# Optimization experiments

Hardware: AMD Instinct MI355X
Metric: run time of the kernel (lower is better)

The kernel has to match this reference:

```python
import jax, jax.numpy as jnp
import numpy as np

NUM_HEADS = 8
WEIGHTS_DIM = 512
INPUT_DIM = 512
D_HEAD = WEIGHTS_DIM // NUM_HEADS


def setup_inputs() -> dict:
    key = jax.random.key(0)
    ks = jax.random.split(key, 9)
    B, S, D = 4, 2048, INPUT_DIM
    s_in = 1.0 / np.sqrt(D)
    s_w = 1.0 / np.sqrt(WEIGHTS_DIM)
    return {
        "x": jax.random.normal(ks[0], (B, S, D), dtype=jnp.float32),
        "Wq": jax.random.normal(ks[1], (D, WEIGHTS_DIM), dtype=jnp.float32) * s_in,
        "bq": jnp.zeros((WEIGHTS_DIM,), dtype=jnp.float32),
        "Wk": jax.random.normal(ks[2], (D, WEIGHTS_DIM), dtype=jnp.float32) * s_in,
        "bk": jnp.zeros((WEIGHTS_DIM,), dtype=jnp.float32),
        "Wv": jax.random.normal(ks[3], (D, WEIGHTS_DIM), dtype=jnp.float32) * s_in,
        "bv": jnp.zeros((WEIGHTS_DIM,), dtype=jnp.float32),
        "Wh": jax.random.normal(ks[4], (WEIGHTS_DIM, D), dtype=jnp.float32) * s_w,
        "bh": jnp.zeros((D,), dtype=jnp.float32),
    }


def _split_heads(t):
    # [B, S, Dm] -> [B, H, S, d_head]
    B, S, _ = t.shape
    return t.reshape(B, S, NUM_HEADS, D_HEAD).transpose(0, 2, 1, 3)


def reference(x, Wq, bq, Wk, bk, Wv, bv, Wh, bh):
    q = _split_heads(x @ Wq + bq)
    k = _split_heads(x @ Wk + bk)
    v = _split_heads(x @ Wv + bv)
    scale = 1.0 / jnp.sqrt(jnp.float32(D_HEAD))
    scores = jnp.einsum("bhqd,bhkd->bhqk", q, k) * scale  # [B,H,S,S]
    weights = jax.nn.softmax(scores, axis=-1)
    attn = jnp.einsum("bhqk,bhkd->bhqd", weights, v)
    B, H, S, d = attn.shape
    concat = attn.transpose(0, 2, 1, 3).reshape(B, S, H * d)
    return concat @ Wh + bh
```

## Files before the change

### kernel.cpp

```cpp
#include <hip/hip_runtime.h>
#include <stdint.h>

#define NB  4
#define SS  2048
#define DD  512
#define HH  8
#define DHH 64
#define MM  (NB * SS)

typedef __attribute__((ext_vector_type(8))) short bf16x8;
typedef __attribute__((ext_vector_type(4))) float f32x4;
typedef __attribute__((ext_vector_type(16))) float f32x16;
typedef __attribute__((ext_vector_type(4))) short s16x4;

union fu32 { float f; unsigned u; };
union pfu  { uint4 u; bf16x8 v; };

static __device__ __forceinline__ short f2bf(float f) {
  fu32 a; a.f = f;
  unsigned u = a.u;
  return (short)((u + 0x7fffu + ((u >> 16) & 1u)) >> 16);
}
static __device__ __forceinline__ float bf2f(short s) {
  fu32 t; t.u = ((unsigned)(unsigned short)s) << 16;
  return t.f;
}

static __device__ __forceinline__ unsigned cvt_pk_bf16(float lo, float hi) {
  unsigned r;
  asm("v_cvt_pk_bf16_f32 %0, %1, %2" : "=v"(r) : "v"(lo), "v"(hi));
  return r;
}
static __device__ __forceinline__ void permlane32_swap(unsigned& a, unsigned& b) {
  asm("v_permlane32_swap_b32 %0, %1" : "+v"(a), "+v"(b));
}

static __device__ __forceinline__ void async16(const void* g, void* l) {
  __builtin_amdgcn_global_load_lds(
      (__attribute__((address_space(1))) unsigned*)(void*)g,
      (__attribute__((address_space(3))) unsigned*)l, 16, 0, 0);
}

__global__ __launch_bounds__(256) void prep_kernel(
    const float* __restrict__ x, short* __restrict__ xb,
    const float* __restrict__ W0, const float* __restrict__ W1,
    const float* __restrict__ W2, const float* __restrict__ W3,
    short* __restrict__ T0, short* __restrict__ T1,
    short* __restrict__ T2, short* __restrict__ T3) {
  const int bid = blockIdx.x, tid = threadIdx.x;
  if (bid < 2048) {
    int i = (bid * 256 + tid) * 8;
    float4 v0 = *(const float4*)(x + i);
    float4 v1 = *(const float4*)(x + i + 4);
    bf16x8 o;
    o[0] = f2bf(v0.x); o[1] = f2bf(v0.y); o[2] = f2bf(v0.z); o[3] = f2bf(v0.w);
    o[4] = f2bf(v1.x); o[5] = f2bf(v1.y); o[6] = f2bf(v1.z); o[7] = f2bf(v1.w);
    *(bf16x8*)(xb + i) = o;
  } else {
    int z = bid - 2048;
    int widx = z >> 6, rem = z & 63;
    const float* W = widx == 0 ? W0 : widx == 1 ? W1 : widx == 2 ? W2 : W3;
    short*       T = widx == 0 ? T0 : widx == 1 ? T1 : widx == 2 ? T2 : T3;
    int n  = (rem & 7) * 64 + (tid & 63);
    int k0 = (rem >> 3) * 64 + (tid >> 6) * 16;
    bf16x8 t0, t1;
#pragma unroll
    for (int j = 0; j < 8; ++j) t0[j] = f2bf(W[(size_t)(k0 + j) * DD + n]);
#pragma unroll
    for (int j = 0; j < 8; ++j) t1[j] = f2bf(W[(size_t)(k0 + 8 + j) * DD + n]);
    *(bf16x8*)(T + (size_t)n * DD + k0)     = t0;
    *(bf16x8*)(T + (size_t)n * DD + k0 + 8) = t1;
  }
}

__global__ __launch_bounds__(256, 4) void gemm_qkv_kernel(
    const short* __restrict__ A, const short* __restrict__ Bt,
    const float* __restrict__ bq, const float* __restrict__ bk,
    const float* __restrict__ bv, short* __restrict__ qout,
    short* __restrict__ kout, short* __restrict__ vtout, float qscale) {
  __shared__ __align__(16) short a_sh[64 * 64];
  __shared__ __align__(16) short b_sh[128 * 64];
  const int tid  = threadIdx.x;
  const int w    = tid >> 6, lane = tid & 63, quad = lane >> 4, l16 = lane & 15;
  const int m0   = blockIdx.y * 64, n0 = blockIdx.x * 128;
  const int mw   = (w >> 1) * 32,   nw = (w & 1) * 64;
  const int rw   = lane >> 3, seg = lane & 7, gs = seg ^ rw;
  const int sxz  = l16 & 7;

  f32x4 acc[2][4];
#pragma unroll
  for (int i = 0; i < 2; ++i)
#pragma unroll
    for (int j = 0; j < 4; ++j) acc[i][j] = {0.f, 0.f, 0.f, 0.f};

  for (int kt = 0; kt < DD; kt += 64) {
    __syncthreads();
    {
      const short* ga = A  + (size_t)(m0 + w * 16 + rw) * DD + kt + gs * 8;
      const short* gb = Bt + (size_t)(n0 + w * 32 + rw) * DD + kt + gs * 8;
#pragma unroll
      for (int i = 0; i < 2; ++i)
        async16(ga + (size_t)i * 8 * DD, &a_sh[(w * 16 + i * 8) * 64]);
#pragma unroll
      for (int i = 0; i < 4; ++i)
        async16(gb + (size_t)i * 8 * DD, &b_sh[(w * 32 + i * 8) * 64]);
    }
    __syncthreads();
#pragma unroll
    for (int ks = 0; ks < 2; ++ks) {
      const int so = ((ks * 4 + quad) ^ sxz) * 8;
      bf16x8 af[2], bfr[4];
#pragma unroll
      for (int mt = 0; mt < 2; ++mt)
        af[mt] = *(const bf16x8*)&a_sh[(mw + mt * 16 + l16) * 64 + so];
#pragma unroll
      for (int nt = 0; nt < 4; ++nt)
        bfr[nt] = *(const bf16x8*)&b_sh[(nw + nt * 16 + l16) * 64 + so];
#pragma unroll
      for (int mt = 0; mt < 2; ++mt)
#pragma unroll
        for (int nt = 0; nt < 4; ++nt)
          acc[mt][nt] = __builtin_amdgcn_mfma_f32_16x16x32_bf16(
              af[mt], bfr[nt], acc[mt][nt], 0, 0, 0);
    }
  }

#pragma unroll
  for (int nt = 0; nt < 4; ++nt) {
    const int n   = n0 + nw + nt * 16 + l16;
    const int sg  = n >> 9, n9 = n & 511, h = n9 >> 6, d = n & 63;
    const float bval = (sg == 0 ? bq : sg == 1 ? bk : bv)[n9];
    const float scl  = (sg == 0) ? qscale : 1.0f;
#pragma unroll
    for (int mt = 0; mt < 2; ++mt) {
      const int mb = m0 + mw + mt * 16 + quad * 4;
      const int bi = mb >> 11, s = mb & (SS - 1);
      if (sg == 2) {
        s16x4 pk;
#pragma unroll
        for (int r = 0; r < 4; ++r) pk[r] = f2bf(acc[mt][nt][r] + bval);
        *(s16x4*)&vtout[((size_t)(bi * HH + h) * DHH + d) * SS + s] = pk;
      } else {
        short* o = (sg == 0) ? qout : kout;
        const size_t base = ((size_t)(bi * HH + h) * SS + s) * DHH + d;
#pragma unroll
        for (int r = 0; r < 4; ++r)
          o[base + (size_t)r * DHH] = f2bf((acc[mt][nt][r] + bval) * scl);
      }
    }
  }
}

__global__ __launch_bounds__(256, 2) void attn_kernel(
    const short* __restrict__ Qa, const short* __restrict__ Ka,
    const short* __restrict__ Vt, short* __restrict__ Op0,
    short* __restrict__ Op1, float* __restrict__ lpw) {
  __shared__ __align__(16) short k_sh[2][64 * 64];
  __shared__ __align__(16) short vt_sh[2][64 * 64];

  const int tid  = threadIdx.x;
  const int w    = tid >> 6, lane = tid & 63;
  const int l32  = lane & 31, hl = lane >> 5;
  const int n    = blockIdx.x;
  const int grp  = (n & 7) * 8 + (n >> 6);
  const int qt_b = (n >> 3) & 7;
  const int half = grp & 1, h = (grp >> 1) & 7, b = grp >> 4;
  const int q0   = qt_b * 256;
  const int rw = lane >> 3, seg = lane & 7, gs = seg ^ rw;
  const size_t base = (size_t)(b * HH + h) * SS * DHH;
  const short* Qg = Qa + base + (size_t)(q0 + w * 64) * DHH;
  const short* Kg = Ka + base;
  const short* Vg = Vt + base;

  bf16x8 qf[2][4];
#pragma unroll
  for (int qx = 0; qx < 2; ++qx)
#pragma unroll
    for (int ds = 0; ds < 4; ++ds)
      qf[qx][ds] = *(const bf16x8*)(Qg + (size_t)(qx * 32 + l32) * DHH + ds * 16 + hl * 8);

  bf16x8 ones;
#pragma unroll
  for (int j = 0; j < 8; ++j) ones[j] = (short)0x3F80;

  f32x16 o_acc[2][2];
  f32x16 l_acc[2];
#pragma unroll
  for (int i = 0; i < 16; ++i) {
    o_acc[0][0][i] = 0.f; o_acc[0][1][i] = 0.f;
    o_acc[1][0][i] = 0.f; o_acc[1][1][i] = 0.f;
    l_acc[0][i] = 0.f; l_acc[1][i] = 0.f;
  }

  const int kstart = half * (SS / 2);
  const int kend   = kstart + SS / 2;

  auto stage = [&](int bsel, int kb) {
    const short* gk = Kg + (size_t)(kb + w * 16 + rw) * DHH + gs * 8;
#pragma unroll
    for (int i = 0; i < 2; ++i)
      async16(gk + (size_t)i * 8 * DHH, &k_sh[bsel][(w * 16 + i * 8) * 64]);
#pragma unroll
    for (int i = 0; i < 2; ++i) {
      const int d = w * 16 + i * 8 + rw;
      async16(Vg + (size_t)d * SS + kb + gs * 8,
              &vt_sh[bsel][(w * 16 + i * 8) * 64]);
    }
  };

  stage(0, kstart);
  __syncthreads();
  int cur = 0;

  for (int kb = kstart; kb < kend; kb += 64) {
    if (kb + 64 < kend) stage(cur ^ 1, kb + 64);

#pragma unroll
    for (int ck = 0; ck < 2; ++ck) {
      const int krow = ck * 32 + l32;
      bf16x8 kf[4];
#pragma unroll
      for (int ds = 0; ds < 4; ++ds) {
        const int sseg = (ds * 2 + hl) ^ (krow & 7);
        kf[ds] = *(const bf16x8*)&k_sh[cur][krow * 64 + sseg * 8];
      }
      f32x16 sarr[2];
#pragma unroll
      for (int qx = 0; qx < 2; ++qx) {
#pragma unroll
        for (int i = 0; i < 16; ++i) sarr[qx][i] = 0.f;
      }
      __builtin_amdgcn_s_setprio(1);
#pragma unroll
      for (int ds = 0; ds < 4; ++ds) {
        sarr[0] = __builtin_amdgcn_mfma_f32_32x32x16_bf16(kf[ds], qf[0][ds], sarr[0], 0, 0, 0);
        sarr[1] = __builtin_amdgcn_mfma_f32_32x32x16_bf16(kf[ds], qf[1][ds], sarr[1], 0, 0, 0);
      }
      __builtin_amdgcn_s_setprio(0);

      pfu a[2][2];
#pragma unroll
      for (int qx = 0; qx < 2; ++qx) {
#pragma unroll
        for (int i = 0; i < 16; ++i) sarr[qx][i] = __builtin_amdgcn_exp2f(sarr[qx][i]);
        unsigned wpk[8];
#pragma unroll
        for (int i = 0; i < 8; ++i)
          wpk[i] = cvt_pk_bf16(sarr[qx][2 * i], sarr[qx][2 * i + 1]);
        permlane32_swap(wpk[0], wpk[2]);
        permlane32_swap(wpk[1], wpk[3]);
        permlane32_swap(wpk[4], wpk[6]);
        permlane32_swap(wpk[5], wpk[7]);
        a[qx][0].u.x = wpk[0]; a[qx][0].u.y = wpk[1];
        a[qx][0].u.z = wpk[2]; a[qx][0].u.w = wpk[3];
        a[qx][1].u.x = wpk[4]; a[qx][1].u.y = wpk[5];
        a[qx][1].u.z = wpk[6]; a[qx][1].u.w = wpk[7];
      }

      __builtin_amdgcn_s_setprio(1);
      l_acc[0] = __builtin_amdgcn_mfma_f32_32x32x16_bf16(a[0][0].v, ones, l_acc[0], 0, 0, 0);
      l_acc[0] = __builtin_amdgcn_mfma_f32_32x32x16_bf16(a[0][1].v, ones, l_acc[0], 0, 0, 0);
      l_acc[1] = __builtin_amdgcn_mfma_f32_32x32x16_bf16(a[1][0].v, ones, l_acc[1], 0, 0, 0);
      l_acc[1] = __builtin_amdgcn_mfma_f32_32x32x16_bf16(a[1][1].v, ones, l_acc[1], 0, 0, 0);

#pragma unroll
      for (int dt = 0; dt < 2; ++dt) {
        const int drow = dt * 32 + l32;
#pragma unroll
        for (int ks = 0; ks < 2; ++ks) {
          const int sseg = (ck * 4 + ks * 2 + hl) ^ (drow & 7);
          bf16x8 vf = *(const bf16x8*)&vt_sh[cur][drow * 64 + sseg * 8];
          o_acc[0][dt] = __builtin_amdgcn_mfma_f32_32x32x16_bf16(
              ks == 0 ? a[0][0].v : a[0][1].v, vf, o_acc[0][dt], 0, 0, 0);
          o_acc[1][dt] = __builtin_amdgcn_mfma_f32_32x32x16_bf16(
              ks == 0 ? a[1][0].v : a[1][1].v, vf, o_acc[1][dt], 0, 0, 0);
        }
      }
      __builtin_amdgcn_s_setprio(0);
    }

    __syncthreads();
    cur ^= 1;
  }

  short* Op = half ? Op1 : Op0;
#pragma unroll
  for (int qx = 0; qx < 2; ++qx) {
#pragma unroll
    for (int r = 0; r < 16; ++r) {
      const int qg = q0 + w * 64 + qx * 32 + (r & 3) + 8 * (r >> 2) + 4 * hl;
      const size_t row = (size_t)(b * HH + h) * SS + qg;
      if (l32 == 0)
        lpw[(size_t)half * (NB * HH * SS) + row] = l_acc[qx][r];
      const float inv = __builtin_amdgcn_rcpf(l_acc[qx][r]);
#pragma unroll
      for (int dt = 0; dt < 2; ++dt)
        Op[row * DHH + dt * 32 + l32] = f2bf(o_acc[qx][dt][r] * inv);
    }
  }
}

__global__ void attn_combine_kernel(const short* __restrict__ Op0,
                                    const short* __restrict__ Op1,
                                    const float* __restrict__ lpw,
                                    short* __restrict__ aws) {
  int idx  = blockIdx.x * 256 + threadIdx.x;
  int dsg  = idx & 7;
  int row  = idx >> 3;
  int q    = row & (SS - 1);
  int bh   = row >> 11, h = bh & 7, b = bh >> 3;
  float l1 = lpw[row], l2 = lpw[NB * HH * SS + row];
  float inv = 1.f / (l1 + l2);
  float w1 = l1 * inv, w2 = l2 * inv;
  bf16x8 a = *(const bf16x8*)&Op0[(size_t)row * DHH + dsg * 8];
  bf16x8 c = *(const bf16x8*)&Op1[(size_t)row * DHH + dsg * 8];
  bf16x8 o;
#pragma unroll
  for (int j = 0; j < 8; ++j) o[j] = f2bf(w1 * bf2f(a[j]) + w2 * bf2f(c[j]));
  *(bf16x8*)&aws[((size_t)(b * SS + q)) * DD + h * DHH + dsg * 8] = o;
}

__global__ __launch_bounds__(256, 4) void gemm_proj_kernel(
    const short* __restrict__ A, const short* __restrict__ Bt,
    const float* __restrict__ bias, float* __restrict__ out) {
  __shared__ __align__(16) short a_sh[64 * 64];
  __shared__ __align__(16) short b_sh[64 * 64];
  const int tid = threadIdx.x;
  const int w   = tid >> 6, lane = tid & 63, quad = lane >> 4, l16 = lane & 15;
  const int m0  = blockIdx.y * 64, n0 = blockIdx.x * 64;
  const int mw  = (w >> 1) * 32, nw = (w & 1) * 32;
  const int rw  = lane >> 3, seg = lane & 7, gs = seg ^ rw;
  const int sxz = l16 & 7;

  f32x4 acc[2][2];
#pragma unroll
  for (int i = 0; i < 2; ++i)
#pragma unroll
    for (int j = 0; j < 2; ++j) acc[i][j] = {0.f, 0.f, 0.f, 0.f};

  for (int kt = 0; kt < DD; kt += 64) {
    __syncthreads();
    {
      const short* ga = A  + (size_t)(m0 + w * 16 + rw) * DD + kt + gs * 8;
      const short* gb = Bt + (size_t)(n0 + w * 16 + rw) * DD + kt + gs * 8;
#pragma unroll
      for (int i = 0; i < 2; ++i) {
        async16(ga + (size_t)i * 8 * DD, &a_sh[(w * 16 + i * 8) * 64]);
        async16(gb + (size_t)i * 8 * DD, &b_sh[(w * 16 + i * 8) * 64]);
      }
    }
    __syncthreads();
#pragma unroll
    for (int ks = 0; ks < 2; ++ks) {
      const int so = ((ks * 4 + quad) ^ sxz) * 8;
      bf16x8 af0 = *(const bf16x8*)&a_sh[(mw + l16) * 64 + so];
      bf16x8 af1 = *(const bf16x8*)&a_sh[(mw + 16 + l16) * 64 + so];
#pragma unroll
      for (int nt = 0; nt < 2; ++nt) {
        bf16x8 bfr = *(const bf16x8*)&b_sh[(nw + nt * 16 + l16) * 64 + so];
        acc[0][nt] = __builtin_amdgcn_mfma_f32_16x16x32_bf16(af0, bfr, acc[0][nt], 0, 0, 0);
        acc[1][nt] = __builtin_amdgcn_mfma_f32_16x16x32_bf16(af1, bfr, acc[1][nt], 0, 0, 0);
      }
    }
  }

#pragma unroll
  for (int nt = 0; nt < 2; ++nt) {
    const int   n  = n0 + nw + nt * 16 + l16;
    const float bv = bias[n];
#pragma unroll
    for (int mt = 0; mt < 2; ++mt)
#pragma unroll
      for (int r = 0; r < 4; ++r) {
        const int m = m0 + mw + mt * 16 + quad * 4 + r;
        out[(size_t)m * DD + n] = acc[mt][nt][r] + bv;
      }
  }
}

extern "C" void kernel_launch(void* const* d_in, const int* in_sizes, int n_in,
                              void* d_out, int out_size, void* d_ws, size_t ws_size,
                              hipStream_t stream) {
  (void)in_sizes; (void)n_in; (void)out_size; (void)ws_size;
  const float* x  = (const float*)d_in[0];
  const float* Wq = (const float*)d_in[1];
  const float* bq = (const float*)d_in[2];
  const float* Wk = (const float*)d_in[3];
  const float* bk = (const float*)d_in[4];
  const float* Wv = (const float*)d_in[5];
  const float* bv = (const float*)d_in[6];
  const float* Wh = (const float*)d_in[7];
  const float* bh = (const float*)d_in[8];

  short* ws  = (short*)d_ws;
  short* xb  = ws;
  short* wqt = xb  + (size_t)MM * DD;
  short* wkt = wqt + (size_t)DD * DD;
  short* wvt = wkt + (size_t)DD * DD;
  short* wht = wvt + (size_t)DD * DD;
  short* qws = wht + (size_t)DD * DD;
  short* kws = qws + (size_t)MM * DD;
  short* vws = kws + (size_t)MM * DD;
  short* aws = vws + (size_t)MM * DD;
  short* op1 = aws + (size_t)MM * DD;
  float* lpw = (float*)(op1 + (size_t)MM * DD);

  hipLaunchKernelGGL(prep_kernel, dim3(2048 + 256), dim3(256), 0, stream,
                     x, xb, Wq, Wk, Wv, Wh, wqt, wkt, wvt, wht);

  const float qscale = 1.4426950408889634f / 8.0f;
  hipLaunchKernelGGL(gemm_qkv_kernel, dim3(12, 128), dim3(256), 0, stream,
                     xb, wqt, bq, bk, bv, qws, kws, vws, qscale);

  hipLaunchKernelGGL(attn_kernel, dim3(512), dim3(256), 0, stream,
                     qws, kws, vws, xb, op1, lpw);
  hipLaunchKernelGGL(attn_combine_kernel, dim3(NB * HH * SS * 8 / 256), dim3(256), 0, stream,
                     xb, op1, lpw, aws);

  hipLaunchKernelGGL(gemm_proj_kernel, dim3(8, 128), dim3(256), 0, stream,
                     aws, wht, bh, (float*)d_out);
}
```

Measured before the change: 166.3 us.

## Split keys across waves within block and fuse split-K combine into attention

Restructures attention so each block handles 64 queries and its four waves each process a quarter of the key range. K/V tiles are read directly from global memory instead of being staged through double-buffered LDS. The partial outputs and row sums are reduced through shared memory, which removes the separate combine kernel and its intermediate buffers. The row-sum MFMAs against a ones vector are replaced with scalar accumulation. The risks are that K/V reuse now depends on cache rather than LDS, and the in-block reduction adds extra LDS traffic and register pressure, with occupancy hinted at 3 blocks per CU.

```diff
diff --git a/kernel.cpp b/kernel.cpp
--- a/kernel.cpp
+++ b/kernel.cpp
@@ -151,24 +151,22 @@
   }
 }
 
-__global__ __launch_bounds__(256, 2) void attn_kernel(
+__global__ __launch_bounds__(256, 3) void attn_kernel(
     const short* __restrict__ Qa, const short* __restrict__ Ka,
-    const short* __restrict__ Vt, short* __restrict__ Op0,
-    short* __restrict__ Op1, float* __restrict__ lpw) {
-  __shared__ __align__(16) short k_sh[2][64 * 64];
-  __shared__ __align__(16) short vt_sh[2][64 * 64];
-
-  const int tid  = threadIdx.x;
-  const int w    = tid >> 6, lane = tid & 63;
-  const int l32  = lane & 31, hl = lane >> 5;
-  const int n    = blockIdx.x;
-  const int grp  = (n & 7) * 8 + (n >> 6);
-  const int qt_b = (n >> 3) & 7;
-  const int half = grp & 1, h = (grp >> 1) & 7, b = grp >> 4;
-  const int q0   = qt_b * 256;
-  const int rw = lane >> 3, seg = lane & 7, gs = seg ^ rw;
+    const short* __restrict__ Vt, short* __restrict__ aws) {
+  __shared__ float Rsh[2][64 * 68];
+  __shared__ float l_sh[4][64];
+
+  const int tid = threadIdx.x;
+  const int w   = tid >> 6, lane = tid & 63;
+  const int l32 = lane & 31, hl = lane >> 5;
+  const int n  = blockIdx.x;
+  const int bh = (n & 7) * 4 + (n >> 8);
+  const int qt = (n >> 3) & 31;
+  const int h  = bh & 7, b = bh >> 3;
+  const int q0 = qt * 64;
   const size_t base = (size_t)(b * HH + h) * SS * DHH;
-  const short* Qg = Qa + base + (size_t)(q0 + w * 64) * DHH;
+  const short* Qg = Qa + base;
   const short* Kg = Ka + base;
   const short* Vg = Vt + base;
 
@@ -177,147 +175,122 @@
   for (int qx = 0; qx < 2; ++qx)
 #pragma unroll
     for (int ds = 0; ds < 4; ++ds)
-      qf[qx][ds] = *(const bf16x8*)(Qg + (size_t)(qx * 32 + l32) * DHH + ds * 16 + hl * 8);
-
-  bf16x8 ones;
-#pragma unroll
-  for (int j = 0; j < 8; ++j) ones[j] = (short)0x3F80;
+      qf[qx][ds] = *(const bf16x8*)(Qg + (size_t)(q0 + qx * 32 + l32) * DHH + ds * 16 + hl * 8);
 
   f32x16 o_acc[2][2];
-  f32x16 l_acc[2];
 #pragma unroll
   for (int i = 0; i < 16; ++i) {
     o_acc[0][0][i] = 0.f; o_acc[0][1][i] = 0.f;
     o_acc[1][0][i] = 0.f; o_acc[1][1][i] = 0.f;
-    l_acc[0][i] = 0.f; l_acc[1][i] = 0.f;
-  }
-
-  const int kstart = half * (SS / 2);
-  const int kend   = kstart + SS / 2;
-
-  auto stage = [&](int bsel, int kb) {
-    const short* gk = Kg + (size_t)(kb + w * 16 + rw) * DHH + gs * 8;
-#pragma unroll
-    for (int i = 0; i < 2; ++i)
-      async16(gk + (size_t)i * 8 * DHH, &k_sh[bsel][(w * 16 + i * 8) * 64]);
-#pragma unroll
-    for (int i = 0; i < 2; ++i) {
-      const int d = w * 16 + i * 8 + rw;
-      async16(Vg + (size_t)d * SS + kb + gs * 8,
-              &vt_sh[bsel][(w * 16 + i * 8) * 64]);
-    }
-  };
-
-  stage(0, kstart);
+  }
+  float lsum0 = 0.f, lsum1 = 0.f;
+
+  const int k0 = w * (SS / 4);
+
+#pragma unroll 2
+  for (int kc = 0; kc < 16; ++kc) {
+    const int kb = k0 + kc * 32;
+    bf16x8 kf[4];
+#pragma unroll
+    for (int ds = 0; ds < 4; ++ds)
+      kf[ds] = *(const bf16x8*)(Kg + (size_t)(kb + l32) * DHH + ds * 16 + hl * 8);
+
+    f32x16 s0, s1;
+#pragma unroll
+    for (int i = 0; i < 16; ++i) { s0[i] = 0.f; s1[i] = 0.f; }
+    __builtin_amdgcn_s_setprio(1);
+#pragma unroll
+    for (int ds = 0; ds < 4; ++ds) {
+      s0 = __builtin_amdgcn_mfma_f32_32x32x16_bf16(kf[ds], qf[0][ds], s0, 0, 0, 0);
+      s1 = __builtin_amdgcn_mfma_f32_32x32x16_bf16(kf[ds], qf[1][ds], s1, 0, 0, 0);
+    }
+    __builtin_amdgcn_s_setprio(0);
+
+    bf16x8 vf[2][2];
+#pragma unroll
+    for (int dt = 0; dt < 2; ++dt)
+#pragma unroll
+      for (int ks = 0; ks < 2; ++ks)
+        vf[dt][ks] = *(const bf16x8*)(Vg + (size_t)(dt * 32 + l32) * SS + kb + ks * 16 + hl * 8);
+
+    pfu a[2][2];
+#pragma unroll
+    for (int qx = 0; qx < 2; ++qx) {
+      f32x16& s = qx ? s1 : s0;
+#pragma unroll
+      for (int i = 0; i < 16; ++i) {
+        s[i] = __builtin_amdgcn_exp2f(s[i]);
+        if (qx) lsum1 += s[i]; else lsum0 += s[i];
+      }
+      unsigned wpk[8];
+#pragma unroll
+      for (int i = 0; i < 8; ++i) wpk[i] = cvt_pk_bf16(s[2 * i], s[2 * i + 1]);
+      permlane32_swap(wpk[0], wpk[2]);
+      permlane32_swap(wpk[1], wpk[3]);
+      permlane32_swap(wpk[4], wpk[6]);
+      permlane32_swap(wpk[5], wpk[7]);
+      a[qx][0].u.x = wpk[0]; a[qx][0].u.y = wpk[1];
+      a[qx][0].u.z = wpk[2]; a[qx][0].u.w = wpk[3];
+      a[qx][1].u.x = wpk[4]; a[qx][1].u.y = wpk[5];
+      a[qx][1].u.z = wpk[6]; a[qx][1].u.w = wpk[7];
+    }
+
+    __builtin_amdgcn_s_setprio(1);
+#pragma unroll
+    for (int dt = 0; dt < 2; ++dt)
+#pragma unroll
+      for (int ks = 0; ks < 2; ++ks) {
+        o_acc[0][dt] = __builtin_amdgcn_mfma_f32_32x32x16_bf16(
+            a[0][ks].v, vf[dt][ks], o_acc[0][dt], 0, 0, 0);
+        o_acc[1][dt] = __builtin_amdgcn_mfma_f32_32x32x16_bf16(
+            a[1][ks].v, vf[dt][ks], o_acc[1][dt], 0, 0, 0);
+      }
+    __builtin_amdgcn_s_setprio(0);
+  }
+
+  lsum0 += __shfl_xor(lsum0, 32);
+  lsum1 += __shfl_xor(lsum1, 32);
+  if (hl == 0) { l_sh[w][l32] = lsum0; l_sh[w][32 + l32] = lsum1; }
+
+  if (w < 2) {
+#pragma unroll
+    for (int qx = 0; qx < 2; ++qx)
+#pragma unroll
+      for (int dt = 0; dt < 2; ++dt)
+#pragma unroll
+        for (int r = 0; r < 16; ++r) {
+          const int qrow = qx * 32 + (r & 3) + 8 * (r >> 2) + 4 * hl;
+          Rsh[w][qrow * 68 + dt * 32 + l32] = o_acc[qx][dt][r];
+        }
+  }
   __syncthreads();
-  int cur = 0;
-
-  for (int kb = kstart; kb < kend; kb += 64) {
-    if (kb + 64 < kend) stage(cur ^ 1, kb + 64);
-
-#pragma unroll
-    for (int ck = 0; ck < 2; ++ck) {
-      const int krow = ck * 32 + l32;
-      bf16x8 kf[4];
-#pragma unroll
-      for (int ds = 0; ds < 4; ++ds) {
-        const int sseg = (ds * 2 + hl) ^ (krow & 7);
-        kf[ds] = *(const bf16x8*)&k_sh[cur][krow * 64 + sseg * 8];
-      }
-      f32x16 sarr[2];
-#pragma unroll
-      for (int qx = 0; qx < 2; ++qx) {
-#pragma unroll
-        for (int i = 0; i < 16; ++i) sarr[qx][i] = 0.f;
-      }
-      __builtin_amdgcn_s_setprio(1);
-#pragma unroll
-      for (int ds = 0; ds < 4; ++ds) {
-        sarr[0] = __builtin_amdgcn_mfma_f32_32x32x16_bf16(kf[ds], qf[0][ds], sarr[0], 0, 0, 0);
-        sarr[1] = __builtin_amdgcn_mfma_f32_32x32x16_bf16(kf[ds], qf[1][ds], sarr[1], 0, 0, 0);
-      }
-      __builtin_amdgcn_s_setprio(0);
-
-      pfu a[2][2];
-#pragma unroll
-      for (int qx = 0; qx < 2; ++qx) {
-#pragma unroll
-        for (int i = 0; i < 16; ++i) sarr[qx][i] = __builtin_amdgcn_exp2f(sarr[qx][i]);
-        unsigned wpk[8];
-#pragma unroll
-        for (int i = 0; i < 8; ++i)
-          wpk[i] = cvt_pk_bf16(sarr[qx][2 * i], sarr[qx][2 * i + 1]);
-        permlane32_swap(wpk[0], wpk[2]);
-        permlane32_swap(wpk[1], wpk[3]);
-        permlane32_swap(wpk[4], wpk[6]);
-        permlane32_swap(wpk[5], wpk[7]);
-        a[qx][0].u.x = wpk[0]; a[qx][0].u.y = wpk[1];
-        a[qx][0].u.z = wpk[2]; a[qx][0].u.w = wpk[3];
-        a[qx][1].u.x = wpk[4]; a[qx][1].u.y = wpk[5];
-        a[qx][1].u.z = wpk[6]; a[qx][1].u.w = wpk[7];
-      }
-
-      __builtin_amdgcn_s_setprio(1);
-      l_acc[0] = __builtin_amdgcn_mfma_f32_32x32x16_bf16(a[0][0].v, ones, l_acc[0], 0, 0, 0);
-      l_acc[0] = __builtin_amdgcn_mfma_f32_32x32x16_bf16(a[0][1].v, ones, l_acc[0], 0, 0, 0);
-      l_acc[1] = __builtin_amdgcn_mfma_f32_32x32x16_bf16(a[1][0].v, ones, l_acc[1], 0, 0, 0);
-      l_acc[1] = __builtin_amdgcn_mfma_f32_32x32x16_bf16(a[1][1].v, ones, l_acc[1], 0, 0, 0);
-
-#pragma unroll
-      for (int dt = 0; dt < 2; ++dt) {
-        const int drow = dt * 32 + l32;
-#pragma unroll
-        for (int ks = 0; ks < 2; ++ks) {
-          const int sseg = (ck * 4 + ks * 2 + hl) ^ (drow & 7);
-          bf16x8 vf = *(const bf16x8*)&vt_sh[cur][drow * 64 + sseg * 8];
-          o_acc[0][dt] = __builtin_amdgcn_mfma_f32_32x32x16_bf16(
-              ks == 0 ? a[0][0].v : a[0][1].v, vf, o_acc[0][dt], 0, 0, 0);
-          o_acc[1][dt] = __builtin_amdgcn_mfma_f32_32x32x16_bf16(
-              ks == 0 ? a[1][0].v : a[1][1].v, vf, o_acc[1][dt], 0, 0, 0);
+  if (w >= 2) {
+#pragma unroll
+    for (int qx = 0; qx < 2; ++qx)
+#pragma unroll
+      for (int dt = 0; dt < 2; ++dt)
+#pragma unroll
+        for (int r = 0; r < 16; ++r) {
+          const int qrow = qx * 32 + (r & 3) + 8 * (r >> 2) + 4 * hl;
+          const int idx  = qrow * 68 + dt * 32 + l32;
+          Rsh[w - 2][idx] += o_acc[qx][dt][r];
         }
-      }
-      __builtin_amdgcn_s_setprio(0);
-    }
-
-    __syncthreads();
-    cur ^= 1;
-  }
-
-  short* Op = half ? Op1 : Op0;
-#pragma unroll
-  for (int qx = 0; qx < 2; ++qx) {
-#pragma unroll
-    for (int r = 0; r < 16; ++r) {
-      const int qg = q0 + w * 64 + qx * 32 + (r & 3) + 8 * (r >> 2) + 4 * hl;
-      const size_t row = (size_t)(b * HH + h) * SS + qg;
-      if (l32 == 0)
-        lpw[(size_t)half * (NB * HH * SS) + row] = l_acc[qx][r];
-      const float inv = __builtin_amdgcn_rcpf(l_acc[qx][r]);
-#pragma unroll
-      for (int dt = 0; dt < 2; ++dt)
-        Op[row * DHH + dt * 32 + l32] = f2bf(o_acc[qx][dt][r] * inv);
-    }
-  }
-}
-
-__global__ void attn_combine_kernel(const short* __restrict__ Op0,
-                                    const short* __restrict__ Op1,
-                                    const float* __restrict__ lpw,
-                                    short* __restrict__ aws) {
-  int idx  = blockIdx.x * 256 + threadIdx.x;
-  int dsg  = idx & 7;
-  int row  = idx >> 3;
-  int q    = row & (SS - 1);
-  int bh   = row >> 11, h = bh & 7, b = bh >> 3;
-  float l1 = lpw[row], l2 = lpw[NB * HH * SS + row];
-  float inv = 1.f / (l1 + l2);
-  float w1 = l1 * inv, w2 = l2 * inv;
-  bf16x8 a = *(const bf16x8*)&Op0[(size_t)row * DHH + dsg * 8];
-  bf16x8 c = *(const bf16x8*)&Op1[(size_t)row * DHH + dsg * 8];
-  bf16x8 o;
-#pragma unroll
-  for (int j = 0; j < 8; ++j) o[j] = f2bf(w1 * bf2f(a[j]) + w2 * bf2f(c[j]));
-  *(bf16x8*)&aws[((size_t)(b * SS + q)) * DD + h * DHH + dsg * 8] = o;
+  }
+  __syncthreads();
+
+  const int q  = tid >> 2;
+  const int dc = (tid & 3) * 16;
+  const float linv = __builtin_amdgcn_rcpf(
+      l_sh[0][q] + l_sh[1][q] + l_sh[2][q] + l_sh[3][q]);
+  bf16x8 o0, o1;
+#pragma unroll
+  for (int j = 0; j < 8; ++j) {
+    o0[j] = f2bf((Rsh[0][q * 68 + dc + j]     + Rsh[1][q * 68 + dc + j])     * linv);
+    o1[j] = f2bf((Rsh[0][q * 68 + dc + 8 + j] + Rsh[1][q * 68 + dc + 8 + j]) * linv);
+  }
+  short* dst = aws + ((size_t)(b * SS + q0 + q)) * DD + h * DHH + dc;
+  *(bf16x8*)dst       = o0;
+  *(bf16x8*)(dst + 8) = o1;
 }
 
 __global__ __launch_bounds__(256, 4) void gemm_proj_kernel(
@@ -402,8 +375,6 @@
   short* kws = qws + (size_t)MM * DD;
   short* vws = kws + (size_t)MM * DD;
   short* aws = vws + (size_t)MM * DD;
-  short* op1 = aws + (size_t)MM * DD;
-  float* lpw = (float*)(op1 + (size_t)MM * DD);
 
   hipLaunchKernelGGL(prep_kernel, dim3(2048 + 256), dim3(256), 0, stream,
                      x, xb, Wq, Wk, Wv, Wh, wqt, wkt, wvt, wht);
@@ -412,10 +383,8 @@
   hipLaunchKernelGGL(gemm_qkv_kernel, dim3(12, 128), dim3(256), 0, stream,
                      xb, wqt, bq, bk, bv, qws, kws, vws, qscale);
 
-  hipLaunchKernelGGL(attn_kernel, dim3(512), dim3(256), 0, stream,
-                     qws, kws, vws, xb, op1, lpw);
-  hipLaunchKernelGGL(attn_combine_kernel, dim3(NB * HH * SS * 8 / 256), dim3(256), 0, stream,
-                     xb, op1, lpw, aws);
+  hipLaunchKernelGGL(attn_kernel, dim3(1024), dim3(256), 0, stream,
+                     qws, kws, vws, aws);
 
   hipLaunchKernelGGL(gemm_proj_kernel, dim3(8, 128), dim3(256), 0, stream,
                      aws, wht, bh, (float*)d_out);
```

Result: slower. 213.3 us (+28.2%).

## Split attention KV range into four partitions and combine four partial outputs

Applied to the files above, without the earlier changes.

The attention kernel now splits each (batch, head, q-tile) KV range into four quarters instead of two. This doubles the grid to 1024 blocks and raises launch bounds to 4 blocks per CU, aiming for better CU occupancy and latency hiding. The combine kernel now merges four normalized partial outputs weighted by their row sums, and the output buffer reuses the V workspace to make room for the extra partials. The cost is more partial-output traffic, a heavier combine step, and tighter register limits that may cause spills.

```diff
diff --git a/kernel.cpp b/kernel.cpp
--- a/kernel.cpp
+++ b/kernel.cpp
@@ -151,10 +151,11 @@
   }
 }
 
-__global__ __launch_bounds__(256, 2) void attn_kernel(
+__global__ __launch_bounds__(256, 4) void attn_kernel(
     const short* __restrict__ Qa, const short* __restrict__ Ka,
     const short* __restrict__ Vt, short* __restrict__ Op0,
-    short* __restrict__ Op1, float* __restrict__ lpw) {
+    short* __restrict__ Op1, short* __restrict__ Op2,
+    short* __restrict__ Op3, float* __restrict__ lpw) {
   __shared__ __align__(16) short k_sh[2][64 * 64];
   __shared__ __align__(16) short vt_sh[2][64 * 64];
 
@@ -162,9 +163,10 @@
   const int w    = tid >> 6, lane = tid & 63;
   const int l32  = lane & 31, hl = lane >> 5;
   const int n    = blockIdx.x;
-  const int grp  = (n & 7) * 8 + (n >> 6);
+  const int grp  = (n & 7) * 16 + (n >> 6);
   const int qt_b = (n >> 3) & 7;
-  const int half = grp & 1, h = (grp >> 1) & 7, b = grp >> 4;
+  const int quarter = grp & 3, bh = grp >> 2;
+  const int h = bh & 7, b = bh >> 3;
   const int q0   = qt_b * 256;
   const int rw = lane >> 3, seg = lane & 7, gs = seg ^ rw;
   const size_t base = (size_t)(b * HH + h) * SS * DHH;
@@ -192,8 +194,8 @@
     l_acc[0][i] = 0.f; l_acc[1][i] = 0.f;
   }
 
-  const int kstart = half * (SS / 2);
-  const int kend   = kstart + SS / 2;
+  const int kstart = quarter * (SS / 4);
+  const int kend   = kstart + SS / 4;
 
   auto stage = [&](int bsel, int kb) {
     const short* gk = Kg + (size_t)(kb + w * 16 + rw) * DHH + gs * 8;
@@ -283,7 +285,7 @@
     cur ^= 1;
   }
 
-  short* Op = half ? Op1 : Op0;
+  short* Op = quarter == 0 ? Op0 : quarter == 1 ? Op1 : quarter == 2 ? Op2 : Op3;
 #pragma unroll
   for (int qx = 0; qx < 2; ++qx) {
 #pragma unroll
@@ -291,7 +293,7 @@
       const int qg = q0 + w * 64 + qx * 32 + (r & 3) + 8 * (r >> 2) + 4 * hl;
       const size_t row = (size_t)(b * HH + h) * SS + qg;
       if (l32 == 0)
-        lpw[(size_t)half * (NB * HH * SS) + row] = l_acc[qx][r];
+        lpw[(size_t)quarter * (NB * HH * SS) + row] = l_acc[qx][r];
       const float inv = __builtin_amdgcn_rcpf(l_acc[qx][r]);
 #pragma unroll
       for (int dt = 0; dt < 2; ++dt)
@@ -302,6 +304,8 @@
 
 __global__ void attn_combine_kernel(const short* __restrict__ Op0,
                                     const short* __restrict__ Op1,
+                                    const short* __restrict__ Op2,
+                                    const short* __restrict__ Op3,
                                     const float* __restrict__ lpw,
                                     short* __restrict__ aws) {
   int idx  = blockIdx.x * 256 + threadIdx.x;
@@ -309,14 +313,20 @@
   int row  = idx >> 3;
   int q    = row & (SS - 1);
   int bh   = row >> 11, h = bh & 7, b = bh >> 3;
-  float l1 = lpw[row], l2 = lpw[NB * HH * SS + row];
-  float inv = 1.f / (l1 + l2);
-  float w1 = l1 * inv, w2 = l2 * inv;
+  const int NR = NB * HH * SS;
+  float l1 = lpw[row],          l2 = lpw[NR + row];
+  float l3 = lpw[2 * NR + row], l4 = lpw[3 * NR + row];
+  float inv = 1.f / (l1 + l2 + l3 + l4);
+  float w1 = l1 * inv, w2 = l2 * inv, w3 = l3 * inv, w4 = l4 * inv;
   bf16x8 a = *(const bf16x8*)&Op0[(size_t)row * DHH + dsg * 8];
   bf16x8 c = *(const bf16x8*)&Op1[(size_t)row * DHH + dsg * 8];
+  bf16x8 d = *(const bf16x8*)&Op2[(size_t)row * DHH + dsg * 8];
+  bf16x8 e = *(const bf16x8*)&Op3[(size_t)row * DHH + dsg * 8];
   bf16x8 o;
 #pragma unroll
-  for (int j = 0; j < 8; ++j) o[j] = f2bf(w1 * bf2f(a[j]) + w2 * bf2f(c[j]));
+  for (int j = 0; j < 8; ++j)
+    o[j] = f2bf(w1 * bf2f(a[j]) + w2 * bf2f(c[j]) +
+                w3 * bf2f(d[j]) + w4 * bf2f(e[j]));
   *(bf16x8*)&aws[((size_t)(b * SS + q)) * DD + h * DHH + dsg * 8] = o;
 }
 
@@ -401,9 +411,11 @@
   short* qws = wht + (size_t)DD * DD;
   short* kws = qws + (size_t)MM * DD;
   short* vws = kws + (size_t)MM * DD;
-  short* aws = vws + (size_t)MM * DD;
-  short* op1 = aws + (size_t)MM * DD;
-  float* lpw = (float*)(op1 + (size_t)MM * DD);
+  short* op1 = vws + (size_t)MM * DD;
+  short* op2 = op1 + (size_t)MM * DD;
+  short* op3 = op2 + (size_t)MM * DD;
+  float* lpw = (float*)(op3 + (size_t)MM * DD);
+  short* aws = vws;
 
   hipLaunchKernelGGL(prep_kernel, dim3(2048 + 256), dim3(256), 0, stream,
                      x, xb, Wq, Wk, Wv, Wh, wqt, wkt, wvt, wht);
@@ -412,10 +424,10 @@
   hipLaunchKernelGGL(gemm_qkv_kernel, dim3(12, 128), dim3(256), 0, stream,
                      xb, wqt, bq, bk, bv, qws, kws, vws, qscale);
 
-  hipLaunchKernelGGL(attn_kernel, dim3(512), dim3(256), 0, stream,
-                     qws, kws, vws, xb, op1, lpw);
+  hipLaunchKernelGGL(attn_kernel, dim3(1024), dim3(256), 0, stream,
+                     qws, kws, vws, xb, op1, op2, op3, lpw);
   hipLaunchKernelGGL(attn_combine_kernel, dim3(NB * HH * SS * 8 / 256), dim3(256), 0, stream,
-                     xb, op1, lpw, aws);
+                     xb, op1, op2, op3, lpw, aws);
 
   hipLaunchKernelGGL(gemm_proj_kernel, dim3(8, 128), dim3(256), 0, stream,
                      aws, wht, bh, (float*)d_out);
```

Result: slower. 410.2 us (+146.7%).
